# Performance work log

Hardware: AMD Instinct MI355X
Metric: run time of the kernel (lower is better)

The kernel has to match this reference:

```python
import jax, jax.numpy as jnp
import numpy as np

B, S, F = 4, 2048, 512
H, DK, DV, FILT = 8, 64, 64, 512

def setup_inputs() -> dict:
    key = jax.random.key(0)
    ks = jax.random.split(key, 11)
    sc_in = 1.0 / np.sqrt(F)
    sc_o = 1.0 / np.sqrt(H * DV)
    return {
        "x_q": jax.random.normal(ks[0], (B, S, F), jnp.float32),
        "x_k": jax.random.normal(ks[1], (B, S, F), jnp.float32),
        "x_v": jax.random.normal(ks[2], (B, S, F), jnp.float32),
        "Wq": jax.random.normal(ks[3], (H, F, DK), jnp.float32) * sc_in,
        "bq": jax.random.normal(ks[4], (H, DK), jnp.float32) * 0.01,
        "Wk": jax.random.normal(ks[5], (H, F, DK), jnp.float32) * sc_in,
        "bk": jax.random.normal(ks[6], (H, DK), jnp.float32) * 0.01,
        "Wv": jax.random.normal(ks[7], (H, F, DV), jnp.float32) * sc_in,
        "bv": jax.random.normal(ks[8], (H, DV), jnp.float32) * 0.01,
        "Wo": jax.random.normal(ks[9], (H * DV, FILT), jnp.float32) * sc_o,
        "bo": jax.random.normal(ks[10], (FILT,), jnp.float32) * 0.01,
    }

def reference(x_q, x_k, x_v, Wq, bq, Wk, bk, Wv, bv, Wo, bo):
    d_k = Wq.shape[-1]
    # per-head Dense projections, batched over heads: [B,H,S,dk/dv]
    q = jnp.einsum("bsf,hfk->bhsk", x_q, Wq) + bq[:, None, :]
    k = jnp.einsum("bsf,hfk->bhsk", x_k, Wk) + bk[:, None, :]
    v = jnp.einsum("bsf,hfv->bhsv", x_v, Wv) + bv[:, None, :]
    # scaled dot-product attention (scale by 1/sqrt(d_k) as in map_fn)
    scores = jnp.einsum("bhsk,bhtk->bhst", q, k) / jnp.sqrt(jnp.asarray(d_k, q.dtype))
    attn = jax.nn.softmax(scores, axis=-1)
    out = jnp.einsum("bhst,bhtv->bhsv", attn, v)
    # concat heads along feature dim -> [B,S,H*DV], then output linear
    bsz, h, s, dv = out.shape
    concat = out.transpose(0, 2, 1, 3).reshape(bsz, s, h * dv)
    return concat @ Wo + bo
```

## Files before the change

kernel.cpp:

```cpp
#include <hip/hip_runtime.h>

#define B_    4
#define S_    2048
#define H_    8
#define M_    (B_ * S_)

typedef __bf16    bf16_t;
typedef _Float16  f16_t;
typedef __bf16   bf16x8 __attribute__((ext_vector_type(8)));
typedef __bf16   bf16x4 __attribute__((ext_vector_type(4)));
typedef _Float16 f16x8  __attribute__((ext_vector_type(8)));
typedef float    f32x16 __attribute__((ext_vector_type(16)));

union B8 { uint4 u; bf16x8 v; bf16_t e[8]; };
union B4 { uint2 u; bf16x4 v; bf16_t e[4]; };
union H8 { uint4 u; f16x8  v; f16_t  e[8]; };
union H4 { uint2 u; f16_t  e[4]; };

#define QSCALE 0.1803368801111204f

__global__ __launch_bounds__(256) void convert_weights(
    const float* __restrict__ w0, const float* __restrict__ w1,
    const float* __restrict__ w2, const float* __restrict__ wo,
    bf16_t* __restrict__ t0, bf16_t* __restrict__ t1,
    bf16_t* __restrict__ t2, f16_t* __restrict__ wot)
{
    __shared__ float T[64][65];
    const int z   = blockIdx.z;
    const int k0  = blockIdx.x * 64;
    const int tid = threadIdx.x;
    const int row = tid & 63, q4 = tid >> 6;

    if (z < 3) {
        const float* W  = z == 0 ? w0 : z == 1 ? w1 : w2;
        bf16_t*      Wt = z == 0 ? t0 : z == 1 ? t1 : t2;
        const int h = blockIdx.y;
        const float* Wh = W + (size_t)h * 512 * 64;
        #pragma unroll
        for (int i = 0; i < 4; ++i) {
            int fq = q4 * 4 + i;
            float4 v = *(const float4*)(Wh + (size_t)(k0 + row) * 64 + fq * 4);
            T[row][fq * 4 + 0] = v.x; T[row][fq * 4 + 1] = v.y;
            T[row][fq * 4 + 2] = v.z; T[row][fq * 4 + 3] = v.w;
        }
        __syncthreads();
        bf16_t* Wth = Wt + (size_t)h * 64 * 512;
        #pragma unroll
        for (int i = 0; i < 4; ++i) {
            int kq = q4 * 4 + i;
            B4 o;
            #pragma unroll
            for (int j = 0; j < 4; ++j) o.e[j] = (bf16_t)T[kq * 4 + j][row];
            *(uint2*)(Wth + (size_t)row * 512 + k0 + kq * 4) = o.u;
        }
    } else {
        const int n0 = blockIdx.y * 64;
        #pragma unroll
        for (int i = 0; i < 4; ++i) {
            int fq = q4 * 4 + i;
            float4 v = *(const float4*)(wo + (size_t)(k0 + row) * 512 + n0 + fq * 4);
            T[row][fq * 4 + 0] = v.x; T[row][fq * 4 + 1] = v.y;
            T[row][fq * 4 + 2] = v.z; T[row][fq * 4 + 3] = v.w;
        }
        __syncthreads();
        #pragma unroll
        for (int i = 0; i < 4; ++i) {
            int kq = q4 * 4 + i;
            H4 o;
            #pragma unroll
            for (int j = 0; j < 4; ++j) o.e[j] = (f16_t)T[kq * 4 + j][row];
            *(uint2*)(wot + (size_t)(n0 + row) * 512 + k0 + kq * 4) = o.u;
        }
    }
}

__global__ __launch_bounds__(256) void proj_tiled(
    const float* __restrict__ xq, const float* __restrict__ xk,
    const float* __restrict__ xv,
    const bf16_t* __restrict__ Wtq, const bf16_t* __restrict__ Wtk,
    const bf16_t* __restrict__ Wtv,
    const float* __restrict__ bq, const float* __restrict__ bk,
    const float* __restrict__ bv,
    bf16_t* __restrict__ Qb, bf16_t* __restrict__ Kb, bf16_t* __restrict__ Vt)
{
    __shared__ bf16_t As[128 * 72];
    __shared__ bf16_t Bs[128 * 72];

    const int z = blockIdx.z;
    const float*  X    = z == 0 ? xq  : z == 1 ? xk  : xv;
    const bf16_t* Wt   = z == 0 ? Wtq : z == 1 ? Wtk : Wtv;
    const float*  bias = z == 0 ? bq  : z == 1 ? bk  : bv;

    const int tid  = threadIdx.x;
    const int wave = tid >> 6, lane = tid & 63;
    const int l31  = lane & 31, half = lane >> 5;
    const int m0   = blockIdx.x * 128;
    const int n0   = blockIdx.y * 128;
    const int mw   = (wave & 1) * 64;
    const int nw   = (wave >> 1) * 64;

    const int sr = tid >> 1;
    const int sc = (tid & 1) * 32;

    float4 ra0[4], ra1[4];
    uint4  rb[4];
    {
        const float*  ap = X  + (size_t)(m0 + sr) * 512 + sc;
        const bf16_t* bp = Wt + (size_t)(n0 + sr) * 512 + sc;
        #pragma unroll
        for (int i = 0; i < 4; ++i) {
            ra0[i] = *(const float4*)(ap + i * 8);
            ra1[i] = *(const float4*)(ap + i * 8 + 4);
            rb[i]  = *(const uint4*)(bp + i * 8);
        }
    }

    f32x16 acc[2][2];
    #pragma unroll
    for (int mt = 0; mt < 2; ++mt)
        #pragma unroll
        for (int nt = 0; nt < 2; ++nt)
            #pragma unroll
            for (int i = 0; i < 16; ++i) acc[mt][nt][i] = 0.0f;

    for (int k0 = 0; k0 < 512; k0 += 64) {
        __syncthreads();
        #pragma unroll
        for (int i = 0; i < 4; ++i) {
            B8 w;
            w.e[0] = (bf16_t)ra0[i].x; w.e[1] = (bf16_t)ra0[i].y;
            w.e[2] = (bf16_t)ra0[i].z; w.e[3] = (bf16_t)ra0[i].w;
            w.e[4] = (bf16_t)ra1[i].x; w.e[5] = (bf16_t)ra1[i].y;
            w.e[6] = (bf16_t)ra1[i].z; w.e[7] = (bf16_t)ra1[i].w;
            *(uint4*)&As[sr * 72 + sc + i * 8] = w.u;
            *(uint4*)&Bs[sr * 72 + sc + i * 8] = rb[i];
        }
        __syncthreads();
        if (k0 + 64 < 512) {
            const float*  ap = X  + (size_t)(m0 + sr) * 512 + k0 + 64 + sc;
            const bf16_t* bp = Wt + (size_t)(n0 + sr) * 512 + k0 + 64 + sc;
            #pragma unroll
            for (int i = 0; i < 4; ++i) {
                ra0[i] = *(const float4*)(ap + i * 8);
                ra1[i] = *(const float4*)(ap + i * 8 + 4);
                rb[i]  = *(const uint4*)(bp + i * 8);
            }
        }

        #pragma unroll
        for (int kc = 0; kc < 4; ++kc) {
            B8 a0, a1, b0, b1;
            a0.u = *(const uint4*)&As[(mw + l31)      * 72 + kc * 16 + half * 8];
            a1.u = *(const uint4*)&As[(mw + 32 + l31) * 72 + kc * 16 + half * 8];
            b0.u = *(const uint4*)&Bs[(nw + l31)      * 72 + kc * 16 + half * 8];
            b1.u = *(const uint4*)&Bs[(nw + 32 + l31) * 72 + kc * 16 + half * 8];
            acc[0][0] = __builtin_amdgcn_mfma_f32_32x32x16_bf16(a0.v, b0.v, acc[0][0], 0, 0, 0);
            acc[0][1] = __builtin_amdgcn_mfma_f32_32x32x16_bf16(a0.v, b1.v, acc[0][1], 0, 0, 0);
            acc[1][0] = __builtin_amdgcn_mfma_f32_32x32x16_bf16(a1.v, b0.v, acc[1][0], 0, 0, 0);
            acc[1][1] = __builtin_amdgcn_mfma_f32_32x32x16_bf16(a1.v, b1.v, acc[1][1], 0, 0, 0);
        }
    }

    if (z <= 1) {
        const float sc_ = (z == 0) ? QSCALE : 1.0f;
        bf16_t* Out = (z == 0) ? Qb : Kb;
        #pragma unroll
        for (int mt = 0; mt < 2; ++mt)
            #pragma unroll
            for (int nt = 0; nt < 2; ++nt) {
                int n = n0 + nw + nt * 32 + l31;
                float bv_ = bias[n];
                #pragma unroll
                for (int r = 0; r < 16; ++r) {
                    int m = m0 + mw + mt * 32 + (r & 3) + 8 * (r >> 2) + 4 * half;
                    Out[(size_t)m * 512 + n] = (bf16_t)((acc[mt][nt][r] + bv_) * sc_);
                }
            }
    } else {
        const int b  = m0 >> 11;
        const int sb = (m0 & 2047);
        #pragma unroll
        for (int mt = 0; mt < 2; ++mt)
            #pragma unroll
            for (int nt = 0; nt < 2; ++nt) {
                int n = n0 + nw + nt * 32 + l31;
                float bv_ = bias[n];
                int h = n >> 6, d = n & 63;
                bf16_t* base = Vt + ((size_t)(b * 8 + h) * 64 + d) * 2048 + sb + mw + mt * 32;
                #pragma unroll
                for (int g = 0; g < 4; ++g) {
                    B4 p;
                    #pragma unroll
                    for (int j = 0; j < 4; ++j) p.e[j] = (bf16_t)(acc[mt][nt][g * 4 + j] + bv_);
                    *(uint2*)(base + 8 * g + 4 * half) = p.u;
                }
            }
    }
}

__global__ __launch_bounds__(512) void attn_mfma(
    const bf16_t* __restrict__ Q, const bf16_t* __restrict__ K,
    const bf16_t* __restrict__ Vt, f16_t* __restrict__ O)
{
    __shared__ char smraw[36864];
    bf16_t* KsBuf = (bf16_t*)smraw;
    bf16_t* VsBuf = KsBuf + 2 * 64 * 72;

    const int bh  = blockIdx.y;
    const int b   = bh >> 3, h = bh & 7;
    const int q0  = blockIdx.x * 128;
    const int tid = threadIdx.x;
    const int wave = tid >> 6, lane = tid & 63;
    const int l31 = lane & 31, half = lane >> 5;
    const int qsub = wave & 3, ksplit = wave >> 2;

    bf16x8 qf[4];
    {
        const bf16_t* qp = Q + ((size_t)(b * S_ + q0 + qsub * 32 + l31)) * 512 + h * 64 + half * 8;
        #pragma unroll
        for (int ks = 0; ks < 4; ++ks) {
            B8 t; t.u = *(const uint4*)(qp + ks * 16);
            qf[ks] = t.v;
        }
    }

    f32x16 o0, o1;
    #pragma unroll
    for (int i = 0; i < 16; ++i) { o0[i] = 0.0f; o1[i] = 0.0f; }
    float l_i = 0.0f;

    const bf16_t* Kbase = K + ((size_t)b * S_) * 512 + h * 64;
    const bf16_t* Vbase = Vt + ((size_t)bh * 64) * 2048;

    const int sbuf = tid >> 8;
    const int p    = tid & 255;
    const int kr = p >> 3, kc8 = p & 7;
    const int vd = p >> 2, vj = p & 3;
    const int kqmap[4] = {0, 2, 1, 3};
    const int vkq = kqmap[vj];
    bf16_t* KsS = KsBuf + sbuf * (64 * 72);
    bf16_t* VsS = VsBuf + sbuf * (64 * 72);
    const bf16_t* KsC = KsBuf + ksplit * (64 * 72);
    const bf16_t* VsC = VsBuf + ksplit * (64 * 72);

    uint4 kreg0, kreg1;
    uint2 vreg[4];
    {
        const int tb = sbuf * 1024;
        kreg0 = *(const uint4*)(Kbase + (size_t)(tb + kr) * 512 + kc8 * 8);
        kreg1 = *(const uint4*)(Kbase + (size_t)(tb + kr + 32) * 512 + kc8 * 8);
        #pragma unroll
        for (int g = 0; g < 4; ++g)
            vreg[g] = *(const uint2*)(Vbase + (size_t)vd * 2048 + tb + g * 16 + vkq * 4);
    }

    for (int t0 = 0; t0 < 1024; t0 += 64) {
        __syncthreads();
        *(uint4*)&KsS[kr * 72 + kc8 * 8]        = kreg0;
        *(uint4*)&KsS[(kr + 32) * 72 + kc8 * 8] = kreg1;
        #pragma unroll
        for (int g = 0; g < 4; ++g)
            *(uint2*)&VsS[vd * 72 + g * 16 + vj * 4] = vreg[g];
        __syncthreads();

        if (t0 + 64 < 1024) {
            const int tb = sbuf * 1024 + t0 + 64;
            kreg0 = *(const uint4*)(Kbase + (size_t)(tb + kr) * 512 + kc8 * 8);
            kreg1 = *(const uint4*)(Kbase + (size_t)(tb + kr + 32) * 512 + kc8 * 8);
            #pragma unroll
            for (int g = 0; g < 4; ++g)
                vreg[g] = *(const uint2*)(Vbase + (size_t)vd * 2048 + tb + g * 16 + vkq * 4);
        }

        f32x16 s0, s1;
        #pragma unroll
        for (int i = 0; i < 16; ++i) { s0[i] = 0.0f; s1[i] = 0.0f; }
        #pragma unroll
        for (int ks = 0; ks < 4; ++ks) {
            B8 k0, k1;
            k0.u = *(const uint4*)(&KsC[l31 * 72 + ks * 16 + half * 8]);
            k1.u = *(const uint4*)(&KsC[(32 + l31) * 72 + ks * 16 + half * 8]);
            s0 = __builtin_amdgcn_mfma_f32_32x32x16_bf16(k0.v, qf[ks], s0, 0, 0, 0);
            s1 = __builtin_amdgcn_mfma_f32_32x32x16_bf16(k1.v, qf[ks], s1, 0, 0, 0);
        }

        float ls = 0.0f;
        #pragma unroll
        for (int r = 0; r < 16; ++r) {
            s0[r] = __builtin_amdgcn_exp2f(s0[r]); ls += s0[r];
            s1[r] = __builtin_amdgcn_exp2f(s1[r]); ls += s1[r];
        }
        l_i += ls;

        B8 pf[4];
        #pragma unroll
        for (int j = 0; j < 8; ++j) {
            pf[0].e[j] = (bf16_t)s0[j];
            pf[1].e[j] = (bf16_t)s0[8 + j];
            pf[2].e[j] = (bf16_t)s1[j];
            pf[3].e[j] = (bf16_t)s1[8 + j];
        }

        #pragma unroll
        for (int c = 0; c < 4; ++c) {
            B8 va, vb;
            va.u = *(const uint4*)(&VsC[l31 * 72 + c * 16 + half * 8]);
            vb.u = *(const uint4*)(&VsC[(32 + l31) * 72 + c * 16 + half * 8]);
            o0 = __builtin_amdgcn_mfma_f32_32x32x16_bf16(va.v, pf[c].v, o0, 0, 0, 0);
            o1 = __builtin_amdgcn_mfma_f32_32x32x16_bf16(vb.v, pf[c].v, o1, 0, 0, 0);
        }
    }

    l_i += __shfl_xor(l_i, 32);
    __syncthreads();
    float* co = (float*)smraw;
    float* cl = co + 4 * 32 * 68;
    if (ksplit == 1) {
        float* reg = co + qsub * (32 * 68);
        #pragma unroll
        for (int r = 0; r < 16; ++r) {
            reg[r * 68 + lane]        = o0[r];
            reg[(16 + r) * 68 + lane] = o1[r];
        }
        cl[qsub * 64 + lane] = l_i;
    }
    __syncthreads();
    if (ksplit == 0) {
        float* reg = co + qsub * (32 * 68);
        float inv = 1.0f / (l_i + cl[qsub * 64 + lane]);
        f16_t* Ob = O + ((size_t)(b * S_ + q0 + qsub * 32 + l31)) * 512 + h * 64;
        #pragma unroll
        for (int g = 0; g < 4; ++g) {
            H4 a, c;
            #pragma unroll
            for (int j = 0; j < 4; ++j) {
                int r = g * 4 + j;
                a.e[j] = (f16_t)((o0[r] + reg[r * 68 + lane]) * inv);
                c.e[j] = (f16_t)((o1[r] + reg[(16 + r) * 68 + lane]) * inv);
            }
            int d = 8 * g + 4 * half;
            *(uint2*)(Ob + d)      = a.u;
            *(uint2*)(Ob + 32 + d) = c.u;
        }
    }
}

__global__ __launch_bounds__(256) void gemm_out_tiled(
    const f16_t* __restrict__ A, const f16_t* __restrict__ Wot,
    const float* __restrict__ bias, float* __restrict__ C)
{
    __shared__ f16_t As[64 * 72];
    __shared__ f16_t Bs[64 * 72];

    const int tid  = threadIdx.x;
    const int wave = tid >> 6, lane = tid & 63;
    const int l31  = lane & 31, half = lane >> 5;
    const int m0   = blockIdx.x * 64;
    const int n0   = blockIdx.y * 64;
    const int mw   = (wave & 1) * 32;
    const int nw   = (wave >> 1) * 32;

    const int sr  = tid >> 2;
    const int so  = (tid & 3) * 16;

    uint4 pA0, pA1, pB0, pB1;
    {
        const f16_t* ap = A   + (size_t)(m0 + sr) * 512 + so;
        const f16_t* bp = Wot + (size_t)(n0 + sr) * 512 + so;
        pA0 = *(const uint4*)(ap); pA1 = *(const uint4*)(ap + 8);
        pB0 = *(const uint4*)(bp); pB1 = *(const uint4*)(bp + 8);
    }

    f32x16 acc;
    #pragma unroll
    for (int i = 0; i < 16; ++i) acc[i] = 0.0f;

    for (int k0 = 0; k0 < 512; k0 += 64) {
        __syncthreads();
        *(uint4*)&As[sr * 72 + so]     = pA0;
        *(uint4*)&As[sr * 72 + so + 8] = pA1;
        *(uint4*)&Bs[sr * 72 + so]     = pB0;
        *(uint4*)&Bs[sr * 72 + so + 8] = pB1;
        __syncthreads();
        if (k0 + 64 < 512) {
            const f16_t* ap = A   + (size_t)(m0 + sr) * 512 + k0 + 64 + so;
            const f16_t* bp = Wot + (size_t)(n0 + sr) * 512 + k0 + 64 + so;
            pA0 = *(const uint4*)(ap); pA1 = *(const uint4*)(ap + 8);
            pB0 = *(const uint4*)(bp); pB1 = *(const uint4*)(bp + 8);
        }

        #pragma unroll
        for (int kc = 0; kc < 4; ++kc) {
            H8 a, b;
            a.u = *(const uint4*)&As[(mw + l31) * 72 + kc * 16 + half * 8];
            b.u = *(const uint4*)&Bs[(nw + l31) * 72 + kc * 16 + half * 8];
            acc = __builtin_amdgcn_mfma_f32_32x32x16_f16(a.v, b.v, acc, 0, 0, 0);
        }
    }

    const int n = n0 + nw + l31;
    const float bias0 = bias[n];
    #pragma unroll
    for (int r = 0; r < 16; ++r) {
        int m = m0 + mw + (r & 3) + 8 * (r >> 2) + 4 * half;
        C[(size_t)m * 512 + n] = acc[r] + bias0;
    }
}

extern "C" void kernel_launch(void* const* d_in, const int* in_sizes, int n_in,
                              void* d_out, int out_size, void* d_ws, size_t ws_size,
                              hipStream_t stream)
{
    const float* x_q = (const float*)d_in[0];
    const float* x_k = (const float*)d_in[1];
    const float* x_v = (const float*)d_in[2];
    const float* Wq  = (const float*)d_in[3];
    const float* bq  = (const float*)d_in[4];
    const float* Wk  = (const float*)d_in[5];
    const float* bk  = (const float*)d_in[6];
    const float* Wv  = (const float*)d_in[7];
    const float* bv  = (const float*)d_in[8];
    const float* Wo  = (const float*)d_in[9];
    const float* bo  = (const float*)d_in[10];
    float* out = (float*)d_out;

    char* W = (char*)d_ws;
    bf16_t* Wtq = (bf16_t*)W;
    bf16_t* Wtk = Wtq + (size_t)8 * 64 * 512;
    bf16_t* Wtv = Wtk + (size_t)8 * 64 * 512;
    f16_t*  Wot = (f16_t*)(Wtv + (size_t)8 * 64 * 512);
    bf16_t* Qb  = (bf16_t*)(Wot + (size_t)512 * 512);
    bf16_t* Kb  = Qb + (size_t)M_ * 512;
    bf16_t* Vt  = Kb + (size_t)M_ * 512;
    f16_t*  AO  = (f16_t*)(Vt + (size_t)M_ * 512);

    convert_weights<<<dim3(8, 8, 4), 256, 0, stream>>>(
        Wq, Wk, Wv, Wo, Wtq, Wtk, Wtv, Wot);

    proj_tiled<<<dim3(64, 4, 3), 256, 0, stream>>>(
        x_q, x_k, x_v, Wtq, Wtk, Wtv, bq, bk, bv, Qb, Kb, Vt);

    attn_mfma<<<dim3(S_ / 128, B_ * H_), 512, 0, stream>>>(Qb, Kb, Vt, AO);

    gemm_out_tiled<<<dim3(128, 8), 256, 0, stream>>>(AO, Wot, bo, out);
}
```

Baseline: 213.8 us.

## Pre-cast inputs to bf16 and stage projection tiles via global_load_lds

```diff
diff --git a/kernel.cpp b/kernel.cpp
--- a/kernel.cpp
+++ b/kernel.cpp
@@ -19,6 +19,32 @@
 
 #define QSCALE 0.1803368801111204f
 
+typedef const __attribute__((address_space(1))) unsigned int ga_u32;
+typedef __attribute__((address_space(3))) unsigned int       ls_u32;
+__device__ __forceinline__ void g2l16(const void* g, void* l) {
+    __builtin_amdgcn_global_load_lds((ga_u32*)g, (ls_u32*)l, 16, 0, 0);
+}
+
+__global__ __launch_bounds__(256) void cast_x(
+    const float* __restrict__ xq, const float* __restrict__ xk,
+    const float* __restrict__ xv,
+    bf16_t* __restrict__ dq, bf16_t* __restrict__ dk, bf16_t* __restrict__ dv)
+{
+    const int z = blockIdx.y;
+    const float* src = z == 0 ? xq : z == 1 ? xk : xv;
+    bf16_t*      dst = z == 0 ? dq : z == 1 ? dk : dv;
+    const size_t base = (size_t)blockIdx.x * 4096 + threadIdx.x * 4;
+    #pragma unroll
+    for (int k = 0; k < 4; ++k) {
+        const size_t i = base + (size_t)k * 1024;
+        float4 v = *(const float4*)(src + i);
+        B4 o;
+        o.e[0] = (bf16_t)v.x; o.e[1] = (bf16_t)v.y;
+        o.e[2] = (bf16_t)v.z; o.e[3] = (bf16_t)v.w;
+        *(uint2*)(dst + i) = o.u;
+    }
+}
+
 __global__ __launch_bounds__(256) void convert_weights(
     const float* __restrict__ w0, const float* __restrict__ w1,
     const float* __restrict__ w2, const float* __restrict__ wo,
@@ -75,19 +101,20 @@
 }
 
 __global__ __launch_bounds__(256) void proj_tiled(
-    const float* __restrict__ xq, const float* __restrict__ xk,
-    const float* __restrict__ xv,
+    const bf16_t* __restrict__ xq, const bf16_t* __restrict__ xk,
+    const bf16_t* __restrict__ xv,
     const bf16_t* __restrict__ Wtq, const bf16_t* __restrict__ Wtk,
     const bf16_t* __restrict__ Wtv,
     const float* __restrict__ bq, const float* __restrict__ bk,
     const float* __restrict__ bv,
     bf16_t* __restrict__ Qb, bf16_t* __restrict__ Kb, bf16_t* __restrict__ Vt)
 {
-    __shared__ bf16_t As[128 * 72];
-    __shared__ bf16_t Bs[128 * 72];
+    __shared__ char sm[34816];
+    bf16_t* As = (bf16_t*)sm;
+    bf16_t* Bs = As + 128 * 64;
 
     const int z = blockIdx.z;
-    const float*  X    = z == 0 ? xq  : z == 1 ? xk  : xv;
+    const bf16_t* X    = z == 0 ? xq  : z == 1 ? xk  : xv;
     const bf16_t* Wt   = z == 0 ? Wtq : z == 1 ? Wtk : Wtv;
     const float*  bias = z == 0 ? bq  : z == 1 ? bk  : bv;
 
@@ -99,21 +126,8 @@
     const int mw   = (wave & 1) * 64;
     const int nw   = (wave >> 1) * 64;
 
-    const int sr = tid >> 1;
-    const int sc = (tid & 1) * 32;
-
-    float4 ra0[4], ra1[4];
-    uint4  rb[4];
-    {
-        const float*  ap = X  + (size_t)(m0 + sr) * 512 + sc;
-        const bf16_t* bp = Wt + (size_t)(n0 + sr) * 512 + sc;
-        #pragma unroll
-        for (int i = 0; i < 4; ++i) {
-            ra0[i] = *(const float4*)(ap + i * 8);
-            ra1[i] = *(const float4*)(ap + i * 8 + 4);
-            rb[i]  = *(const uint4*)(bp + i * 8);
-        }
-    }
+    const int srow = lane >> 3;
+    const int scol = (lane & 7) * 16;
 
     f32x16 acc[2][2];
     #pragma unroll
@@ -127,33 +141,22 @@
         __syncthreads();
         #pragma unroll
         for (int i = 0; i < 4; ++i) {
-            B8 w;
-            w.e[0] = (bf16_t)ra0[i].x; w.e[1] = (bf16_t)ra0[i].y;
-            w.e[2] = (bf16_t)ra0[i].z; w.e[3] = (bf16_t)ra0[i].w;
-            w.e[4] = (bf16_t)ra1[i].x; w.e[5] = (bf16_t)ra1[i].y;
-            w.e[6] = (bf16_t)ra1[i].z; w.e[7] = (bf16_t)ra1[i].w;
-            *(uint4*)&As[sr * 72 + sc + i * 8] = w.u;
-            *(uint4*)&Bs[sr * 72 + sc + i * 8] = rb[i];
-        }
-        __syncthreads();
-        if (k0 + 64 < 512) {
-            const float*  ap = X  + (size_t)(m0 + sr) * 512 + k0 + 64 + sc;
-            const bf16_t* bp = Wt + (size_t)(n0 + sr) * 512 + k0 + 64 + sc;
-            #pragma unroll
-            for (int i = 0; i < 4; ++i) {
-                ra0[i] = *(const float4*)(ap + i * 8);
-                ra1[i] = *(const float4*)(ap + i * 8 + 4);
-                rb[i]  = *(const uint4*)(bp + i * 8);
-            }
-        }
+            const int inst = wave * 4 + i;
+            const int row  = inst * 8 + srow;
+            g2l16((const char*)X  + ((size_t)(m0 + row) * 512 + k0) * 2 + scol,
+                  sm + inst * 1024);
+            g2l16((const char*)Wt + ((size_t)(n0 + row) * 512 + k0) * 2 + scol,
+                  sm + 16384 + inst * 1024);
+        }
+        __syncthreads();
 
         #pragma unroll
         for (int kc = 0; kc < 4; ++kc) {
             B8 a0, a1, b0, b1;
-            a0.u = *(const uint4*)&As[(mw + l31)      * 72 + kc * 16 + half * 8];
-            a1.u = *(const uint4*)&As[(mw + 32 + l31) * 72 + kc * 16 + half * 8];
-            b0.u = *(const uint4*)&Bs[(nw + l31)      * 72 + kc * 16 + half * 8];
-            b1.u = *(const uint4*)&Bs[(nw + 32 + l31) * 72 + kc * 16 + half * 8];
+            a0.u = *(const uint4*)&As[(mw + l31)      * 64 + kc * 16 + half * 8];
+            a1.u = *(const uint4*)&As[(mw + 32 + l31) * 64 + kc * 16 + half * 8];
+            b0.u = *(const uint4*)&Bs[(nw + l31)      * 64 + kc * 16 + half * 8];
+            b1.u = *(const uint4*)&Bs[(nw + 32 + l31) * 64 + kc * 16 + half * 8];
             acc[0][0] = __builtin_amdgcn_mfma_f32_32x32x16_bf16(a0.v, b0.v, acc[0][0], 0, 0, 0);
             acc[0][1] = __builtin_amdgcn_mfma_f32_32x32x16_bf16(a0.v, b1.v, acc[0][1], 0, 0, 0);
             acc[1][0] = __builtin_amdgcn_mfma_f32_32x32x16_bf16(a1.v, b0.v, acc[1][0], 0, 0, 0);
@@ -178,23 +181,34 @@
             }
     } else {
         const int b  = m0 >> 11;
-        const int sb = (m0 & 2047);
+        const int sb = m0 & 2047;
+        __syncthreads();
         #pragma unroll
         for (int mt = 0; mt < 2; ++mt)
             #pragma unroll
             for (int nt = 0; nt < 2; ++nt) {
-                int n = n0 + nw + nt * 32 + l31;
-                float bv_ = bias[n];
-                int h = n >> 6, d = n & 63;
-                bf16_t* base = Vt + ((size_t)(b * 8 + h) * 64 + d) * 2048 + sb + mw + mt * 32;
+                const int nl  = nw + nt * 32 + l31;
+                const float bv_ = bias[n0 + nl];
                 #pragma unroll
-                for (int g = 0; g < 4; ++g) {
-                    B4 p;
-                    #pragma unroll
-                    for (int j = 0; j < 4; ++j) p.e[j] = (bf16_t)(acc[mt][nt][g * 4 + j] + bv_);
-                    *(uint2*)(base + 8 * g + 4 * half) = p.u;
+                for (int r = 0; r < 16; r += 2) {
+                    const int ml = mw + mt * 32 + (r & 3) + 8 * (r >> 2) + 4 * half;
+                    union { unsigned u; bf16_t e[2]; } pk;
+                    pk.e[0] = (bf16_t)(acc[mt][nt][r]     + bv_);
+                    pk.e[1] = (bf16_t)(acc[mt][nt][r + 1] + bv_);
+                    *(unsigned*)(sm + nl * 272 + ml * 2) = pk.u;
                 }
             }
+        __syncthreads();
+        const int dl16 = tid >> 4;
+        const int cc   = tid & 15;
+        #pragma unroll
+        for (int p = 0; p < 8; ++p) {
+            const int d_l = p * 16 + dl16;
+            const int ng  = n0 + d_l;
+            const int h   = ng >> 6, dd = ng & 63;
+            uint4 val = *(const uint4*)(sm + d_l * 272 + cc * 16);
+            *(uint4*)(Vt + ((size_t)((b * 8 + h) * 64 + dd)) * 2048 + sb + cc * 8) = val;
+        }
     }
 }
 
@@ -434,11 +448,17 @@
     bf16_t* Vt  = Kb + (size_t)M_ * 512;
     f16_t*  AO  = (f16_t*)(Vt + (size_t)M_ * 512);
 
+    bf16_t* Xqb = (bf16_t*)out;
+    bf16_t* Xkb = Xqb + (size_t)M_ * 512;
+    bf16_t* Xvb = (bf16_t*)AO;
+
+    cast_x<<<dim3(1024, 3), 256, 0, stream>>>(x_q, x_k, x_v, Xqb, Xkb, Xvb);
+
     convert_weights<<<dim3(8, 8, 4), 256, 0, stream>>>(
         Wq, Wk, Wv, Wo, Wtq, Wtk, Wtv, Wot);
 
     proj_tiled<<<dim3(64, 4, 3), 256, 0, stream>>>(
-        x_q, x_k, x_v, Wtq, Wtk, Wtv, bq, bk, bv, Qb, Kb, Vt);
+        Xqb, Xkb, Xvb, Wtq, Wtk, Wtv, bq, bk, bv, Qb, Kb, Vt);
 
     attn_mfma<<<dim3(S_ / 128, B_ * H_), 512, 0, stream>>>(Qb, Kb, Vt, AO);
 
```

Result: faster. 202.8 us (-5.2%).
